# Kernel tuning notes

Measured on AMD Instinct MI355X. Metric: run time of the kernel, lower is better.

## Reference

```python
import jax, jax.numpy as jnp
import numpy as np

B, N_EX, N_KC, D_E, D_C, D_H = 32, 1024, 128, 64, 64, 64


def setup_inputs() -> dict:
    key = jax.random.key(0)
    ks = jax.random.split(key, 20)
    return {
        "h": jax.random.normal(ks[0], (B, N_KC, D_H), jnp.float32),
        "ex": jax.random.uniform(ks[1], (B, N_EX), jnp.float32),
        "su": jax.random.uniform(ks[2], (B,), jnp.float32),
        "ex_graph": jax.random.uniform(ks[3], (N_EX, N_KC), jnp.float32),
        "kc_gamma": jax.random.normal(ks[4], (N_KC, N_KC), jnp.float32),
        "W_ex": jax.random.normal(ks[5], (D_E, 2 * N_EX), jnp.float32) * 0.02,
        "W_kc": jax.random.normal(ks[6], (D_C, N_KC), jnp.float32) * 0.05,
        "tgru_wih": jax.random.normal(ks[7], (3 * D_H, D_E), jnp.float32) * 0.05,
        "tgru_whh": jax.random.normal(ks[8], (3 * D_H, D_H), jnp.float32) * 0.05,
        "tgru_bih": jax.random.normal(ks[9], (3 * D_H,), jnp.float32) * 0.05,
        "tgru_bhh": jax.random.normal(ks[10], (3 * D_H,), jnp.float32) * 0.05,
        "fpart_w": jax.random.normal(ks[11], (D_H, D_C + D_H), jnp.float32) * 0.05,
        "fpart_b": jax.random.normal(ks[12], (D_H,), jnp.float32) * 0.05,
        "ulin_w": jax.random.normal(ks[13], (D_H, D_H), jnp.float32) * 0.05,
        "ulin_b": jax.random.normal(ks[14], (D_H,), jnp.float32) * 0.05,
        "ugru_wih": jax.random.normal(ks[15], (3 * D_H, D_H), jnp.float32) * 0.05,
        "ugru_whh": jax.random.normal(ks[16], (3 * D_H, D_H), jnp.float32) * 0.05,
        "ugru_bih": jax.random.normal(ks[17], (3 * D_H,), jnp.float32) * 0.05,
        "ugru_bhh": jax.random.normal(ks[18], (3 * D_H,), jnp.float32) * 0.05,
    }


def _gru_cell(x, h, wih, whh, bih, bhh):
    # torch.nn.GRUCell: gates in order r, z, n
    gi = x @ wih.T + bih
    gh = h @ whh.T + bhh
    ir, iz, inn = jnp.split(gi, 3, axis=-1)
    hr, hz, hn = jnp.split(gh, 3, axis=-1)
    r = jax.nn.sigmoid(ir + hr)
    z = jax.nn.sigmoid(iz + hz)
    n = jnp.tanh(inn + r * hn)
    return (1.0 - z) * n + z * h


def reference(h, ex, su, ex_graph, kc_gamma, W_ex, W_kc,
              tgru_wih, tgru_whh, tgru_bih, tgru_bhh,
              fpart_w, fpart_b, ulin_w, ulin_b,
              ugru_wih, ugru_whh, ugru_bih, ugru_bhh):
    bsz, n_kc, d_h = h.shape
    kc_graph = jax.nn.sigmoid(kc_gamma)  # (n_kc, n_kc)

    # exercise embedding from [ex*su, ex*(1-su)]
    x_id = jnp.concatenate([ex * su[:, None], ex * (1.0 - su)[:, None]], axis=-1)  # (B, 2*n_ex)
    x = x_id @ W_ex.T  # (B, d_e)

    kci = ex @ ex_graph  # (B, n_kc)
    kci_flat = kci.reshape(bsz * n_kc, 1)

    # temporal GRU update, gated by kci
    x_rep = jnp.broadcast_to(x[:, None, :], (bsz, n_kc, x.shape[-1])).reshape(bsz * n_kc, -1)
    h_flat = h.reshape(bsz * n_kc, d_h)
    th = _gru_cell(x_rep, h_flat, tgru_wih, tgru_whh, tgru_bih, tgru_bhh)
    new_h = (1.0 - kci_flat) * h_flat + kci_flat * th  # (B*n_kc, d_h)

    delta_h = (new_h - h_flat).reshape(bsz, n_kc, d_h)

    # kc_embeddings(eye(n_kc)) == W_kc.T : (n_kc, d_c)
    e = W_kc.T
    # fpart(concat([delta_h_i, e_j])) split into the two weight blocks
    W_dh = fpart_w[:, :d_h]   # acts on delta_h
    W_e = fpart_w[:, d_h:]    # acts on e
    dpart = delta_h @ W_dh.T                      # (B, n_kc_i, d_h)
    epart = e @ W_e.T + fpart_b                   # (n_kc_j, d_h)
    pre = dpart[:, :, None, :] + epart[None, None, :, :]  # (B, i, j, d_h)
    partij = jax.nn.relu(pre)
    partij = partij * kc_graph[None, :, :, None] * kci[:, :, None, None]
    partj = jnp.sum(partij, axis=1)               # (B, n_kc_j, d_h)

    outj = jax.nn.relu(partj @ ulin_w.T + ulin_b).reshape(bsz * n_kc, d_h)
    kcj = (kci @ kc_graph).reshape(bsz * n_kc, 1)

    uh = _gru_cell(outj, new_h, ugru_wih, ugru_whh, ugru_bih, ugru_bhh)
    h_out = (1.0 - kcj) * new_h + kcj * uh
    return h_out.reshape(bsz, n_kc, d_h)
```

## Files before the change

### kernel.cpp

```cpp
#include <hip/hip_runtime.h>
#include <math.h>

#define NB  32
#define NKC 128
#define DH  64
#define NEX 1024
#define G3  192

#define XOFF    0
#define KCIOFF  2048
#define DPOFF   6144
#define FLAGOFF 268288
#define FLAGBYTE (FLAGOFF * 4)

#define S_WHH   0
#define S_WIH   6912
#define S_HT    13824
#define S_DLT   14848
#define S_XS    15872
#define S_KRED  15936
#define S_GIS   16448
#define S_BHH3  16640
#define S_KCIL  16832
#define S_DPT   0
#define S_FWB   8448
#define S_WKT   12800
#define S_PJS   13888
#define S_OUTJ  14912
#define S_EPS   15936
#define S_NEWH  17024
#define S_KCIF  18048
#define S_KCJ   18176
#define S_BIH   18192
#define S_BHH   18384
#define SM_SIZE 18576

__device__ __forceinline__ float sigf(float x) { return 1.0f / (1.0f + expf(-x)); }
__device__ __forceinline__ float dot4(float4 a, float4 b) {
    return fmaf(a.x, b.x, fmaf(a.y, b.y, fmaf(a.z, b.z, a.w * b.w)));
}

__global__ __launch_bounds__(512) void kF(
    const float* __restrict__ h, const float* __restrict__ ex,
    const float* __restrict__ su, const float* __restrict__ ex_graph,
    const float* __restrict__ kc_gamma,
    const float* __restrict__ W_ex, const float* __restrict__ W_kc,
    const float* __restrict__ tgru_wih, const float* __restrict__ tgru_whh,
    const float* __restrict__ tgru_bih, const float* __restrict__ tgru_bhh,
    const float* __restrict__ fpart_w, const float* __restrict__ fpart_b,
    const float* __restrict__ ulin_w, const float* __restrict__ ulin_b,
    const float* __restrict__ ugru_wih, const float* __restrict__ ugru_whh,
    const float* __restrict__ ugru_bih, const float* __restrict__ ugru_bhh,
    float* __restrict__ ws, float* __restrict__ out)
{
    int t = threadIdx.x, wave = t >> 6, lane = t & 63;
    int b  = blockIdx.x >> 3;
    int ck = blockIdx.x & 7;
    int i0 = ck * 16;

    __shared__ __align__(16) float sm[SM_SIZE];
    int* fx = (int*)(ws + FLAGOFF);
    int* fd = fx + 32;

    {
        float sub = su[b];
        const float* exb = ex + (size_t)b * NEX;
        float er[16];
        #pragma unroll
        for (int i = 0; i < 16; ++i) er[i] = exb[lane + i * 64];
        int d = ck * 8 + wave;
        const float* wr = W_ex + (size_t)d * (2 * NEX);
        float a1 = 0.f, a2 = 0.f;
        #pragma unroll
        for (int i = 0; i < 16; ++i) {
            int k = lane + i * 64;
            a1 = fmaf(er[i], wr[k], a1);
            a2 = fmaf(er[i], wr[NEX + k], a2);
        }
        float v = sub * a1 + (1.0f - sub) * a2;
        #pragma unroll
        for (int off = 32; off; off >>= 1) v += __shfl_down(v, off, 64);
        if (lane == 0) ws[XOFF + b * DH + d] = v;
    }
    __syncthreads();
    if (t == 0)
        __hip_atomic_fetch_add(fx + b, 1, __ATOMIC_RELEASE, __HIP_MEMORY_SCOPE_AGENT);

    {
        int i = t & 15, ks = t >> 4, kb = ks * 32;
        const float* exb = ex + (size_t)b * NEX;
        const float* eg = ex_graph + i0 + i;
        float a = 0.f;
        #pragma unroll 4
        for (int k = 0; k < 32; ++k)
            a = fmaf(exb[kb + k], eg[(size_t)(kb + k) * NKC], a);
        sm[S_KRED + t] = a;
    }
    {
        const float* hb = h + (size_t)(b * NKC + i0) * DH;
        for (int idx = t; idx < 16 * DH; idx += 512) sm[S_HT + idx] = hb[idx];
    }
    if (t < G3) sm[S_BHH3 + t] = tgru_bhh[t];
    __syncthreads();
    if (t < 16) {
        float s = 0.f;
        #pragma unroll
        for (int r = 0; r < 32; ++r) s += sm[S_KRED + r * 16 + t];
        sm[S_KCIL + t] = s;
        ws[KCIOFF + b * NKC + i0 + t] = s;
    }
    if (t == 0) {
        while (__hip_atomic_load(fx + b, __ATOMIC_ACQUIRE, __HIP_MEMORY_SCOPE_AGENT) < 8)
            __builtin_amdgcn_s_sleep(1);
    }
    __syncthreads();
    if (t < DH) sm[S_XS + t] = ws[XOFF + b * DH + t];

    float giA = (t < G3) ? tgru_bih[t] : 0.f;
    float ar[2], az[2], an[2];
    #pragma unroll
    for (int m = 0; m < 2; ++m) {
        ar[m] = sm[S_BHH3 + lane];
        az[m] = sm[S_BHH3 + 64 + lane];
        an[m] = sm[S_BHH3 + 128 + lane];
    }
    for (int ch = 0; ch < 2; ++ch) {
        __syncthreads();
        for (int idx = t; idx < G3 * 8; idx += 512) {
            int row = idx >> 3, q = idx & 7;
            *(float4*)&sm[S_WHH + row * 36 + 4 * q] =
                *(const float4*)&tgru_whh[row * DH + ch * 32 + 4 * q];
            *(float4*)&sm[S_WIH + row * 36 + 4 * q] =
                *(const float4*)&tgru_wih[row * DH + ch * 32 + 4 * q];
        }
        __syncthreads();
        if (t < G3) {
            #pragma unroll
            for (int q = 0; q < 8; ++q) {
                float4 wv = *(float4*)&sm[S_WIH + t * 36 + 4 * q];
                float4 xv = *(float4*)&sm[S_XS + ch * 32 + 4 * q];
                giA += dot4(wv, xv);
            }
        }
        #pragma unroll
        for (int q = 0; q < 8; ++q) {
            float4 wr = *(float4*)&sm[S_WHH + lane * 36 + 4 * q];
            float4 wz = *(float4*)&sm[S_WHH + (64 + lane) * 36 + 4 * q];
            float4 wn = *(float4*)&sm[S_WHH + (128 + lane) * 36 + 4 * q];
            int kb2 = ch * 32 + 4 * q;
            #pragma unroll
            for (int m = 0; m < 2; ++m) {
                float4 hk = *(float4*)&sm[S_HT + (wave * 2 + m) * DH + kb2];
                ar[m] += dot4(wr, hk);
                az[m] += dot4(wz, hk);
                an[m] += dot4(wn, hk);
            }
        }
    }
    if (t < G3) sm[S_GIS + t] = giA;
    __syncthreads();
    #pragma unroll
    for (int m = 0; m < 2; ++m) {
        int il = wave * 2 + m;
        float hval = sm[S_HT + il * DH + lane];
        float r = sigf(sm[S_GIS + lane] + ar[m]);
        float z = sigf(sm[S_GIS + 64 + lane] + az[m]);
        float n = tanhf(sm[S_GIS + 128 + lane] + r * an[m]);
        float th = (1.0f - z) * n + z * hval;
        float kv = sm[S_KCIL + il];
        float nh = (1.0f - kv) * hval + kv * th;
        sm[S_NEWH + il * DH + lane] = nh;
        sm[S_DLT + il * DH + lane] = kv * (th - hval);
    }
    __syncthreads();
    for (int idx = t; idx < 64 * 16; idx += 512) {
        int d = idx >> 4, q = idx & 15;
        *(float4*)&sm[S_WHH + d * 68 + 4 * q] = *(const float4*)&fpart_w[d * 128 + 4 * q];
    }
    __syncthreads();
    float acc[2] = {0.f, 0.f};
    #pragma unroll
    for (int q = 0; q < 16; ++q) {
        float4 w = *(float4*)&sm[S_WHH + lane * 68 + 4 * q];
        #pragma unroll
        for (int m = 0; m < 2; ++m) {
            float4 dv = *(float4*)&sm[S_DLT + (wave * 2 + m) * DH + 4 * q];
            acc[m] += dot4(w, dv);
        }
    }
    __syncthreads();
    #pragma unroll
    for (int m = 0; m < 2; ++m) sm[S_WIH + lane * 17 + wave * 2 + m] = acc[m];
    __syncthreads();
    for (int idx = t; idx < 1024; idx += 512) {
        int d = idx >> 4, il = idx & 15;
        ws[DPOFF + (size_t)b * 8192 + d * NKC + i0 + il] = sm[S_WIH + d * 17 + il];
    }
    __syncthreads();
    if (t == 0)
        __hip_atomic_fetch_add(fd + b, 1, __ATOMIC_RELEASE, __HIP_MEMORY_SCOPE_AGENT);

    for (int idx = t; idx < 64 * 16; idx += 512) {
        int d = idx >> 4, q = idx & 15;
        *(float4*)&sm[S_FWB + d * 68 + 4 * q] =
            *(const float4*)&fpart_w[d * 128 + 64 + 4 * q];
    }
    for (int idx = t; idx < 1024; idx += 512) {
        int cc = idx >> 4, jl = idx & 15;
        sm[S_WKT + jl * 68 + cc] = W_kc[(size_t)cc * NKC + i0 + jl];
    }
    if (t < G3) { sm[S_BIH + t] = ugru_bih[t]; sm[S_BHH + t] = ugru_bhh[t]; }
    if (t == 0) {
        while (__hip_atomic_load(fd + b, __ATOMIC_ACQUIRE, __HIP_MEMORY_SCOPE_AGENT) < 8)
            __builtin_amdgcn_s_sleep(1);
    }
    __syncthreads();
    {
        const float* dp = ws + DPOFF + (size_t)b * 8192;
        #pragma unroll
        for (int r = 0; r < 4; ++r) {
            int idx4 = t + r * 512;
            int d = idx4 >> 5, qi = idx4 & 31;
            *(float4*)&sm[S_DPT + d * 132 + 4 * qi] = *(const float4*)&dp[d * NKC + 4 * qi];
        }
    }
    if (t < NKC) sm[S_KCIF + t] = ws[KCIOFF + b * NKC + t];
    __syncthreads();
    #pragma unroll
    for (int r = 0; r < 2; ++r) {
        int idx = t + r * 512;
        int jl = idx >> 6, d = idx & 63;
        float a = fpart_b[d];
        #pragma unroll
        for (int q = 0; q < 16; ++q) {
            float4 fv = *(float4*)&sm[S_FWB + d * 68 + 4 * q];
            float4 wv = *(float4*)&sm[S_WKT + jl * 68 + 4 * q];
            a += dot4(fv, wv);
        }
        sm[S_EPS + jl * DH + d] = a;
    }
    __syncthreads();
    for (int idx = t; idx < 2048; idx += 512) {
        int i = idx >> 4, jl = idx & 15;
        sm[S_FWB + jl * 132 + i] = sm[S_KCIF + i] * sigf(kc_gamma[i * NKC + i0 + jl]);
    }
    __syncthreads();
    if (t < 16) {
        float s = 0.f;
        #pragma unroll
        for (int qi = 0; qi < 32; ++qi) {
            float4 v = *(float4*)&sm[S_FWB + t * 132 + 4 * qi];
            s += v.x + v.y + v.z + v.w;
        }
        sm[S_KCJ + t] = s;
    }
    float ep[2], pa[2];
    #pragma unroll
    for (int m = 0; m < 2; ++m) {
        ep[m] = sm[S_EPS + (wave * 2 + m) * DH + lane];
        pa[m] = 0.f;
    }
    for (int qi = 0; qi < 32; ++qi) {
        float4 dv = *(float4*)&sm[S_DPT + lane * 132 + 4 * qi];
        #pragma unroll
        for (int m = 0; m < 2; ++m) {
            float4 wv = *(float4*)&sm[S_FWB + (wave * 2 + m) * 132 + 4 * qi];
            pa[m] = fmaf(fmaxf(dv.x + ep[m], 0.f), wv.x, pa[m]);
            pa[m] = fmaf(fmaxf(dv.y + ep[m], 0.f), wv.y, pa[m]);
            pa[m] = fmaf(fmaxf(dv.z + ep[m], 0.f), wv.z, pa[m]);
            pa[m] = fmaf(fmaxf(dv.w + ep[m], 0.f), wv.w, pa[m]);
        }
    }
    #pragma unroll
    for (int m = 0; m < 2; ++m) sm[S_PJS + (wave * 2 + m) * DH + lane] = pa[m];
    __syncthreads();
    for (int idx = t; idx < 64 * 16; idx += 512) {
        int d = idx >> 4, q = idx & 15;
        *(float4*)&sm[d * 68 + 4 * q] = *(const float4*)&ulin_w[d * DH + 4 * q];
    }
    float ulb = ulin_b[lane];
    __syncthreads();
    float oa[2] = {ulb, ulb};
    #pragma unroll
    for (int q = 0; q < 16; ++q) {
        float4 uv = *(float4*)&sm[lane * 68 + 4 * q];
        #pragma unroll
        for (int m = 0; m < 2; ++m) {
            float4 pv = *(float4*)&sm[S_PJS + (wave * 2 + m) * DH + 4 * q];
            oa[m] += dot4(uv, pv);
        }
    }
    #pragma unroll
    for (int m = 0; m < 2; ++m)
        sm[S_OUTJ + (wave * 2 + m) * DH + lane] = fmaxf(oa[m], 0.f);
    float gir[2], giz[2], gin[2], ghr[2], ghz[2], ghn[2];
    #pragma unroll
    for (int m = 0; m < 2; ++m)
        gir[m] = giz[m] = gin[m] = ghr[m] = ghz[m] = ghn[m] = 0.f;
    for (int ch = 0; ch < 2; ++ch) {
        __syncthreads();
        for (int idx = t; idx < G3 * 8; idx += 512) {
            int row = idx >> 3, q = idx & 7;
            *(float4*)&sm[row * 36 + 4 * q] =
                *(const float4*)&ugru_wih[row * DH + ch * 32 + 4 * q];
            *(float4*)&sm[6912 + row * 36 + 4 * q] =
                *(const float4*)&ugru_whh[row * DH + ch * 32 + 4 * q];
        }
        __syncthreads();
        #pragma unroll
        for (int q = 0; q < 8; ++q) {
            float4 wir = *(float4*)&sm[lane * 36 + 4 * q];
            float4 wiz = *(float4*)&sm[(64 + lane) * 36 + 4 * q];
            float4 win = *(float4*)&sm[(128 + lane) * 36 + 4 * q];
            float4 wwr = *(float4*)&sm[6912 + lane * 36 + 4 * q];
            float4 wwz = *(float4*)&sm[6912 + (64 + lane) * 36 + 4 * q];
            float4 wwn = *(float4*)&sm[6912 + (128 + lane) * 36 + 4 * q];
            int kb2 = ch * 32 + 4 * q;
            #pragma unroll
            for (int m = 0; m < 2; ++m) {
                int jl = wave * 2 + m;
                float4 ov = *(float4*)&sm[S_OUTJ + jl * DH + kb2];
                float4 nv = *(float4*)&sm[S_NEWH + jl * DH + kb2];
                gir[m] += dot4(wir, ov);
                giz[m] += dot4(wiz, ov);
                gin[m] += dot4(win, ov);
                ghr[m] += dot4(wwr, nv);
                ghz[m] += dot4(wwz, nv);
                ghn[m] += dot4(wwn, nv);
            }
        }
    }
    #pragma unroll
    for (int m = 0; m < 2; ++m) {
        int jl = wave * 2 + m;
        float r = sigf(gir[m] + sm[S_BIH + lane] + ghr[m] + sm[S_BHH + lane]);
        float z = sigf(giz[m] + sm[S_BIH + 64 + lane] + ghz[m] + sm[S_BHH + 64 + lane]);
        float n = tanhf(gin[m] + sm[S_BIH + 128 + lane] +
                        r * (ghn[m] + sm[S_BHH + 128 + lane]));
        float nh = sm[S_NEWH + jl * DH + lane];
        float uh = (1.0f - z) * n + z * nh;
        float kj = sm[S_KCJ + jl];
        out[(size_t)(b * NKC + i0 + jl) * DH + lane] = (1.0f - kj) * nh + kj * uh;
    }
}

extern "C" void kernel_launch(void* const* d_in, const int* in_sizes, int n_in,
                              void* d_out, int out_size, void* d_ws, size_t ws_size,
                              hipStream_t stream) {
    const float* h        = (const float*)d_in[0];
    const float* ex       = (const float*)d_in[1];
    const float* su       = (const float*)d_in[2];
    const float* ex_graph = (const float*)d_in[3];
    const float* kc_gamma = (const float*)d_in[4];
    const float* W_ex     = (const float*)d_in[5];
    const float* W_kc     = (const float*)d_in[6];
    const float* tgru_wih = (const float*)d_in[7];
    const float* tgru_whh = (const float*)d_in[8];
    const float* tgru_bih = (const float*)d_in[9];
    const float* tgru_bhh = (const float*)d_in[10];
    const float* fpart_w  = (const float*)d_in[11];
    const float* fpart_b  = (const float*)d_in[12];
    const float* ulin_w   = (const float*)d_in[13];
    const float* ulin_b   = (const float*)d_in[14];
    const float* ugru_wih = (const float*)d_in[15];
    const float* ugru_whh = (const float*)d_in[16];
    const float* ugru_bih = (const float*)d_in[17];
    const float* ugru_bhh = (const float*)d_in[18];
    float* ws  = (float*)d_ws;
    float* out = (float*)d_out;

    hipMemsetAsync((char*)d_ws + FLAGBYTE, 0, 64 * sizeof(int), stream);
    hipLaunchKernelGGL(kF, dim3(256), dim3(512), 0, stream,
                       h, ex, su, ex_graph, kc_gamma, W_ex, W_kc,
                       tgru_wih, tgru_whh, tgru_bih, tgru_bhh,
                       fpart_w, fpart_b, ulin_w, ulin_b,
                       ugru_wih, ugru_whh, ugru_bih, ugru_bhh,
                       ws, out);
}
```

Measured before the change: 134.6 us.

## Split each batch into 16 blocks of 8 KCs, doubling grid size

The fused kernel now launches 512 blocks, each owning 8 knowledge components instead of 16, so every wave handles a single row rather than two. The change is meant to spread work across more of the MI355X's compute units and shorten each block's serial per-row work. It also moves kc_gamma, fpart_b and ulin_b loads ahead of the spin-wait, reworks the kci reduction into two stages, and compacts the shared-memory layout. In exchange, every block reloads all GRU and fpart weights, which doubles that global traffic. The per-batch spin barriers also now wait on 16 blocks, which requires all of them to be co-resident.

```diff
diff --git a/kernel.cpp b/kernel.cpp
--- a/kernel.cpp
+++ b/kernel.cpp
@@ -6,6 +6,8 @@
 #define DH  64
 #define NEX 1024
 #define G3  192
+#define CHK 8
+#define NCK 16
 
 #define XOFF    0
 #define KCIOFF  2048
@@ -14,33 +16,39 @@
 #define FLAGBYTE (FLAGOFF * 4)
 
 #define S_WHH   0
-#define S_WIH   6912
-#define S_HT    13824
-#define S_DLT   14848
-#define S_XS    15872
-#define S_KRED  15936
-#define S_GIS   16448
-#define S_BHH3  16640
-#define S_KCIL  16832
 #define S_DPT   0
+#define S_UL    0
+#define S_WIH36 0
+#define S_WHH36 6912
+#define S_WIH   8448
+#define S_DPTT  8448
 #define S_FWB   8448
+#define S_WJT   8448
 #define S_WKT   12800
-#define S_PJS   13888
-#define S_OUTJ  14912
-#define S_EPS   15936
-#define S_NEWH  17024
-#define S_KCIF  18048
-#define S_KCJ   18176
-#define S_BIH   18192
-#define S_BHH   18384
-#define SM_SIZE 18576
+#define S_HT    15360
+#define S_PJS   15360
+#define S_DLT   15872
+#define S_OUTJ  15872
+#define S_XS    16384
+#define S_KRED  16448
+#define S_EPS   16448
+#define S_KR2   16960
+#define S_GIS   17024
+#define S_BHH3  17216
+#define S_KCIL  17408
+#define S_NEWH  17424
+#define S_KCIF  17936
+#define S_KCJ   18064
+#define S_BIH   18080
+#define S_BHH   18272
+#define SM_SIZE 18464
 
 __device__ __forceinline__ float sigf(float x) { return 1.0f / (1.0f + expf(-x)); }
 __device__ __forceinline__ float dot4(float4 a, float4 b) {
     return fmaf(a.x, b.x, fmaf(a.y, b.y, fmaf(a.z, b.z, a.w * b.w)));
 }
 
-__global__ __launch_bounds__(512) void kF(
+__global__ __launch_bounds__(512, 4) void kF(
     const float* __restrict__ h, const float* __restrict__ ex,
     const float* __restrict__ su, const float* __restrict__ ex_graph,
     const float* __restrict__ kc_gamma,
@@ -54,21 +62,21 @@
     float* __restrict__ ws, float* __restrict__ out)
 {
     int t = threadIdx.x, wave = t >> 6, lane = t & 63;
-    int b  = blockIdx.x >> 3;
-    int ck = blockIdx.x & 7;
-    int i0 = ck * 16;
+    int b  = blockIdx.x >> 4;
+    int ck = blockIdx.x & 15;
+    int i0 = ck * CHK;
 
     __shared__ __align__(16) float sm[SM_SIZE];
     int* fx = (int*)(ws + FLAGOFF);
     int* fd = fx + 32;
 
-    {
+    if (wave < 4) {
         float sub = su[b];
         const float* exb = ex + (size_t)b * NEX;
         float er[16];
         #pragma unroll
         for (int i = 0; i < 16; ++i) er[i] = exb[lane + i * 64];
-        int d = ck * 8 + wave;
+        int d = ck * 4 + wave;
         const float* wr = W_ex + (size_t)d * (2 * NEX);
         float a1 = 0.f, a2 = 0.f;
         #pragma unroll
@@ -82,48 +90,51 @@
         for (int off = 32; off; off >>= 1) v += __shfl_down(v, off, 64);
         if (lane == 0) ws[XOFF + b * DH + d] = v;
     }
+    {
+        int i = t & 7, ks = t >> 3, kb = ks * 16;
+        const float* exb = ex + (size_t)b * NEX;
+        const float* eg = ex_graph + i0 + i;
+        float a0 = 0.f, a1 = 0.f;
+        #pragma unroll
+        for (int k = 0; k < 16; k += 2) {
+            a0 = fmaf(exb[kb + k],     eg[(size_t)(kb + k) * NKC], a0);
+            a1 = fmaf(exb[kb + k + 1], eg[(size_t)(kb + k + 1) * NKC], a1);
+        }
+        sm[S_KRED + t] = a0 + a1;
+    }
+    if (t < 128) {
+        const float* hb = h + (size_t)(b * NKC + i0) * DH;
+        *(float4*)&sm[S_HT + t * 4] = *(const float4*)&hb[t * 4];
+    }
+    if (t < G3) sm[S_BHH3 + t] = tgru_bhh[t];
     __syncthreads();
     if (t == 0)
         __hip_atomic_fetch_add(fx + b, 1, __ATOMIC_RELEASE, __HIP_MEMORY_SCOPE_AGENT);
-
-    {
-        int i = t & 15, ks = t >> 4, kb = ks * 32;
-        const float* exb = ex + (size_t)b * NEX;
-        const float* eg = ex_graph + i0 + i;
-        float a = 0.f;
-        #pragma unroll 4
-        for (int k = 0; k < 32; ++k)
-            a = fmaf(exb[kb + k], eg[(size_t)(kb + k) * NKC], a);
-        sm[S_KRED + t] = a;
-    }
-    {
-        const float* hb = h + (size_t)(b * NKC + i0) * DH;
-        for (int idx = t; idx < 16 * DH; idx += 512) sm[S_HT + idx] = hb[idx];
-    }
-    if (t < G3) sm[S_BHH3 + t] = tgru_bhh[t];
-    __syncthreads();
-    if (t < 16) {
+    if (t < 64) {
+        int i = t & 7, r = t >> 3;
         float s = 0.f;
         #pragma unroll
-        for (int r = 0; r < 32; ++r) s += sm[S_KRED + r * 16 + t];
+        for (int q = 0; q < 8; ++q) s += sm[S_KRED + (r * 8 + q) * 8 + i];
+        sm[S_KR2 + t] = s;
+    }
+    if (t < 8) {
+        float s = 0.f;
+        #pragma unroll
+        for (int q = 0; q < 8; ++q) s += sm[S_KR2 + q * 8 + t];
         sm[S_KCIL + t] = s;
         ws[KCIOFF + b * NKC + i0 + t] = s;
     }
     if (t == 0) {
-        while (__hip_atomic_load(fx + b, __ATOMIC_ACQUIRE, __HIP_MEMORY_SCOPE_AGENT) < 8)
+        while (__hip_atomic_load(fx + b, __ATOMIC_ACQUIRE, __HIP_MEMORY_SCOPE_AGENT) < NCK)
             __builtin_amdgcn_s_sleep(1);
     }
     __syncthreads();
     if (t < DH) sm[S_XS + t] = ws[XOFF + b * DH + t];
 
     float giA = (t < G3) ? tgru_bih[t] : 0.f;
-    float ar[2], az[2], an[2];
-    #pragma unroll
-    for (int m = 0; m < 2; ++m) {
-        ar[m] = sm[S_BHH3 + lane];
-        az[m] = sm[S_BHH3 + 64 + lane];
-        an[m] = sm[S_BHH3 + 128 + lane];
-    }
+    float ar = sm[S_BHH3 + lane];
+    float az = sm[S_BHH3 + 64 + lane];
+    float an = sm[S_BHH3 + 128 + lane];
     for (int ch = 0; ch < 2; ++ch) {
         __syncthreads();
         for (int idx = t; idx < G3 * 8; idx += 512) {
@@ -136,41 +147,31 @@
         __syncthreads();
         if (t < G3) {
             #pragma unroll
-            for (int q = 0; q < 8; ++q) {
-                float4 wv = *(float4*)&sm[S_WIH + t * 36 + 4 * q];
-                float4 xv = *(float4*)&sm[S_XS + ch * 32 + 4 * q];
-                giA += dot4(wv, xv);
-            }
+            for (int q = 0; q < 8; ++q)
+                giA += dot4(*(float4*)&sm[S_WIH + t * 36 + 4 * q],
+                            *(float4*)&sm[S_XS + ch * 32 + 4 * q]);
         }
         #pragma unroll
         for (int q = 0; q < 8; ++q) {
-            float4 wr = *(float4*)&sm[S_WHH + lane * 36 + 4 * q];
-            float4 wz = *(float4*)&sm[S_WHH + (64 + lane) * 36 + 4 * q];
-            float4 wn = *(float4*)&sm[S_WHH + (128 + lane) * 36 + 4 * q];
             int kb2 = ch * 32 + 4 * q;
-            #pragma unroll
-            for (int m = 0; m < 2; ++m) {
-                float4 hk = *(float4*)&sm[S_HT + (wave * 2 + m) * DH + kb2];
-                ar[m] += dot4(wr, hk);
-                az[m] += dot4(wz, hk);
-                an[m] += dot4(wn, hk);
-            }
+            float4 hk = *(float4*)&sm[S_HT + wave * DH + kb2];
+            ar += dot4(*(float4*)&sm[S_WHH + lane * 36 + 4 * q], hk);
+            az += dot4(*(float4*)&sm[S_WHH + (64 + lane) * 36 + 4 * q], hk);
+            an += dot4(*(float4*)&sm[S_WHH + (128 + lane) * 36 + 4 * q], hk);
         }
     }
     if (t < G3) sm[S_GIS + t] = giA;
     __syncthreads();
-    #pragma unroll
-    for (int m = 0; m < 2; ++m) {
-        int il = wave * 2 + m;
-        float hval = sm[S_HT + il * DH + lane];
-        float r = sigf(sm[S_GIS + lane] + ar[m]);
-        float z = sigf(sm[S_GIS + 64 + lane] + az[m]);
-        float n = tanhf(sm[S_GIS + 128 + lane] + r * an[m]);
+    {
+        float hval = sm[S_HT + wave * DH + lane];
+        float r = sigf(sm[S_GIS + lane] + ar);
+        float z = sigf(sm[S_GIS + 64 + lane] + az);
+        float n = tanhf(sm[S_GIS + 128 + lane] + r * an);
         float th = (1.0f - z) * n + z * hval;
-        float kv = sm[S_KCIL + il];
+        float kv = sm[S_KCIL + wave];
         float nh = (1.0f - kv) * hval + kv * th;
-        sm[S_NEWH + il * DH + lane] = nh;
-        sm[S_DLT + il * DH + lane] = kv * (th - hval);
+        sm[S_NEWH + wave * DH + lane] = nh;
+        sm[S_DLT + wave * DH + lane] = kv * (th - hval);
     }
     __syncthreads();
     for (int idx = t; idx < 64 * 16; idx += 512) {
@@ -178,40 +179,38 @@
         *(float4*)&sm[S_WHH + d * 68 + 4 * q] = *(const float4*)&fpart_w[d * 128 + 4 * q];
     }
     __syncthreads();
-    float acc[2] = {0.f, 0.f};
+    float acc = 0.f;
     #pragma unroll
-    for (int q = 0; q < 16; ++q) {
-        float4 w = *(float4*)&sm[S_WHH + lane * 68 + 4 * q];
-        #pragma unroll
-        for (int m = 0; m < 2; ++m) {
-            float4 dv = *(float4*)&sm[S_DLT + (wave * 2 + m) * DH + 4 * q];
-            acc[m] += dot4(w, dv);
-        }
-    }
-    __syncthreads();
-    #pragma unroll
-    for (int m = 0; m < 2; ++m) sm[S_WIH + lane * 17 + wave * 2 + m] = acc[m];
-    __syncthreads();
-    for (int idx = t; idx < 1024; idx += 512) {
-        int d = idx >> 4, il = idx & 15;
-        ws[DPOFF + (size_t)b * 8192 + d * NKC + i0 + il] = sm[S_WIH + d * 17 + il];
+    for (int q = 0; q < 16; ++q)
+        acc += dot4(*(float4*)&sm[S_WHH + lane * 68 + 4 * q],
+                    *(float4*)&sm[S_DLT + wave * DH + 4 * q]);
+    sm[S_DPTT + lane * 9 + wave] = acc;
+    __syncthreads();
+    {
+        int d = t >> 3, il = t & 7;
+        ws[DPOFF + (size_t)b * 8192 + d * NKC + i0 + il] = sm[S_DPTT + d * 9 + il];
     }
     __syncthreads();
     if (t == 0)
         __hip_atomic_fetch_add(fd + b, 1, __ATOMIC_RELEASE, __HIP_MEMORY_SCOPE_AGENT);
 
+    int ic = t >> 3, jc = t & 7;
+    float g0  = kc_gamma[(size_t)ic * NKC + i0 + jc];
+    float g1  = kc_gamma[(size_t)(ic + 64) * NKC + i0 + jc];
+    float fpb = fpart_b[t & 63];
+    float ulb = ulin_b[lane];
     for (int idx = t; idx < 64 * 16; idx += 512) {
         int d = idx >> 4, q = idx & 15;
         *(float4*)&sm[S_FWB + d * 68 + 4 * q] =
             *(const float4*)&fpart_w[d * 128 + 64 + 4 * q];
     }
-    for (int idx = t; idx < 1024; idx += 512) {
-        int cc = idx >> 4, jl = idx & 15;
-        sm[S_WKT + jl * 68 + cc] = W_kc[(size_t)cc * NKC + i0 + jl];
+    {
+        int c = t >> 3, jl = t & 7;
+        sm[S_WKT + jl * 68 + c] = W_kc[(size_t)c * NKC + i0 + jl];
     }
     if (t < G3) { sm[S_BIH + t] = ugru_bih[t]; sm[S_BHH + t] = ugru_bhh[t]; }
     if (t == 0) {
-        while (__hip_atomic_load(fd + b, __ATOMIC_ACQUIRE, __HIP_MEMORY_SCOPE_AGENT) < 8)
+        while (__hip_atomic_load(fd + b, __ATOMIC_ACQUIRE, __HIP_MEMORY_SCOPE_AGENT) < NCK)
             __builtin_amdgcn_s_sleep(1);
     }
     __syncthreads();
@@ -226,121 +225,83 @@
     }
     if (t < NKC) sm[S_KCIF + t] = ws[KCIOFF + b * NKC + t];
     __syncthreads();
-    #pragma unroll
-    for (int r = 0; r < 2; ++r) {
-        int idx = t + r * 512;
-        int jl = idx >> 6, d = idx & 63;
-        float a = fpart_b[d];
-        #pragma unroll
-        for (int q = 0; q < 16; ++q) {
-            float4 fv = *(float4*)&sm[S_FWB + d * 68 + 4 * q];
-            float4 wv = *(float4*)&sm[S_WKT + jl * 68 + 4 * q];
-            a += dot4(fv, wv);
-        }
+    {
+        int jl = t >> 6, d = t & 63;
+        float a = fpb;
+        #pragma unroll
+        for (int q = 0; q < 16; ++q)
+            a += dot4(*(float4*)&sm[S_FWB + d * 68 + 4 * q],
+                      *(float4*)&sm[S_WKT + jl * 68 + 4 * q]);
         sm[S_EPS + jl * DH + d] = a;
     }
     __syncthreads();
-    for (int idx = t; idx < 2048; idx += 512) {
-        int i = idx >> 4, jl = idx & 15;
-        sm[S_FWB + jl * 132 + i] = sm[S_KCIF + i] * sigf(kc_gamma[i * NKC + i0 + jl]);
-    }
-    __syncthreads();
-    if (t < 16) {
+    sm[S_WJT + jc * 132 + ic]      = sm[S_KCIF + ic]      * sigf(g0);
+    sm[S_WJT + jc * 132 + ic + 64] = sm[S_KCIF + ic + 64] * sigf(g1);
+    __syncthreads();
+    if (t < 8) {
         float s = 0.f;
         #pragma unroll
         for (int qi = 0; qi < 32; ++qi) {
-            float4 v = *(float4*)&sm[S_FWB + t * 132 + 4 * qi];
+            float4 v = *(float4*)&sm[S_WJT + t * 132 + 4 * qi];
             s += v.x + v.y + v.z + v.w;
         }
         sm[S_KCJ + t] = s;
     }
-    float ep[2], pa[2];
-    #pragma unroll
-    for (int m = 0; m < 2; ++m) {
-        ep[m] = sm[S_EPS + (wave * 2 + m) * DH + lane];
-        pa[m] = 0.f;
-    }
+    float ep = sm[S_EPS + wave * DH + lane], pa = 0.f;
     for (int qi = 0; qi < 32; ++qi) {
         float4 dv = *(float4*)&sm[S_DPT + lane * 132 + 4 * qi];
-        #pragma unroll
-        for (int m = 0; m < 2; ++m) {
-            float4 wv = *(float4*)&sm[S_FWB + (wave * 2 + m) * 132 + 4 * qi];
-            pa[m] = fmaf(fmaxf(dv.x + ep[m], 0.f), wv.x, pa[m]);
-            pa[m] = fmaf(fmaxf(dv.y + ep[m], 0.f), wv.y, pa[m]);
-            pa[m] = fmaf(fmaxf(dv.z + ep[m], 0.f), wv.z, pa[m]);
-            pa[m] = fmaf(fmaxf(dv.w + ep[m], 0.f), wv.w, pa[m]);
-        }
-    }
-    #pragma unroll
-    for (int m = 0; m < 2; ++m) sm[S_PJS + (wave * 2 + m) * DH + lane] = pa[m];
+        float4 wv = *(float4*)&sm[S_WJT + wave * 132 + 4 * qi];
+        pa = fmaf(fmaxf(dv.x + ep, 0.f), wv.x, pa);
+        pa = fmaf(fmaxf(dv.y + ep, 0.f), wv.y, pa);
+        pa = fmaf(fmaxf(dv.z + ep, 0.f), wv.z, pa);
+        pa = fmaf(fmaxf(dv.w + ep, 0.f), wv.w, pa);
+    }
+    sm[S_PJS + wave * DH + lane] = pa;
     __syncthreads();
     for (int idx = t; idx < 64 * 16; idx += 512) {
         int d = idx >> 4, q = idx & 15;
-        *(float4*)&sm[d * 68 + 4 * q] = *(const float4*)&ulin_w[d * DH + 4 * q];
-    }
-    float ulb = ulin_b[lane];
-    __syncthreads();
-    float oa[2] = {ulb, ulb};
+        *(float4*)&sm[S_UL + d * 68 + 4 * q] = *(const float4*)&ulin_w[d * DH + 4 * q];
+    }
+    __syncthreads();
+    float oa = ulb;
     #pragma unroll
-    for (int q = 0; q < 16; ++q) {
-        float4 uv = *(float4*)&sm[lane * 68 + 4 * q];
-        #pragma unroll
-        for (int m = 0; m < 2; ++m) {
-            float4 pv = *(float4*)&sm[S_PJS + (wave * 2 + m) * DH + 4 * q];
-            oa[m] += dot4(uv, pv);
-        }
-    }
-    #pragma unroll
-    for (int m = 0; m < 2; ++m)
-        sm[S_OUTJ + (wave * 2 + m) * DH + lane] = fmaxf(oa[m], 0.f);
-    float gir[2], giz[2], gin[2], ghr[2], ghz[2], ghn[2];
-    #pragma unroll
-    for (int m = 0; m < 2; ++m)
-        gir[m] = giz[m] = gin[m] = ghr[m] = ghz[m] = ghn[m] = 0.f;
+    for (int q = 0; q < 16; ++q)
+        oa += dot4(*(float4*)&sm[S_UL + lane * 68 + 4 * q],
+                   *(float4*)&sm[S_PJS + wave * DH + 4 * q]);
+    sm[S_OUTJ + wave * DH + lane] = fmaxf(oa, 0.f);
+    float gir = 0.f, giz = 0.f, gin = 0.f, ghr = 0.f, ghz = 0.f, ghn = 0.f;
     for (int ch = 0; ch < 2; ++ch) {
         __syncthreads();
         for (int idx = t; idx < G3 * 8; idx += 512) {
             int row = idx >> 3, q = idx & 7;
-            *(float4*)&sm[row * 36 + 4 * q] =
+            *(float4*)&sm[S_WIH36 + row * 36 + 4 * q] =
                 *(const float4*)&ugru_wih[row * DH + ch * 32 + 4 * q];
-            *(float4*)&sm[6912 + row * 36 + 4 * q] =
+            *(float4*)&sm[S_WHH36 + row * 36 + 4 * q] =
                 *(const float4*)&ugru_whh[row * DH + ch * 32 + 4 * q];
         }
         __syncthreads();
         #pragma unroll
         for (int q = 0; q < 8; ++q) {
-            float4 wir = *(float4*)&sm[lane * 36 + 4 * q];
-            float4 wiz = *(float4*)&sm[(64 + lane) * 36 + 4 * q];
-            float4 win = *(float4*)&sm[(128 + lane) * 36 + 4 * q];
-            float4 wwr = *(float4*)&sm[6912 + lane * 36 + 4 * q];
-            float4 wwz = *(float4*)&sm[6912 + (64 + lane) * 36 + 4 * q];
-            float4 wwn = *(float4*)&sm[6912 + (128 + lane) * 36 + 4 * q];
             int kb2 = ch * 32 + 4 * q;
-            #pragma unroll
-            for (int m = 0; m < 2; ++m) {
-                int jl = wave * 2 + m;
-                float4 ov = *(float4*)&sm[S_OUTJ + jl * DH + kb2];
-                float4 nv = *(float4*)&sm[S_NEWH + jl * DH + kb2];
-                gir[m] += dot4(wir, ov);
-                giz[m] += dot4(wiz, ov);
-                gin[m] += dot4(win, ov);
-                ghr[m] += dot4(wwr, nv);
-                ghz[m] += dot4(wwz, nv);
-                ghn[m] += dot4(wwn, nv);
-            }
-        }
-    }
-    #pragma unroll
-    for (int m = 0; m < 2; ++m) {
-        int jl = wave * 2 + m;
-        float r = sigf(gir[m] + sm[S_BIH + lane] + ghr[m] + sm[S_BHH + lane]);
-        float z = sigf(giz[m] + sm[S_BIH + 64 + lane] + ghz[m] + sm[S_BHH + 64 + lane]);
-        float n = tanhf(gin[m] + sm[S_BIH + 128 + lane] +
-                        r * (ghn[m] + sm[S_BHH + 128 + lane]));
-        float nh = sm[S_NEWH + jl * DH + lane];
+            float4 ov = *(float4*)&sm[S_OUTJ + wave * DH + kb2];
+            float4 nv = *(float4*)&sm[S_NEWH + wave * DH + kb2];
+            gir += dot4(*(float4*)&sm[S_WIH36 + lane * 36 + 4 * q], ov);
+            giz += dot4(*(float4*)&sm[S_WIH36 + (64 + lane) * 36 + 4 * q], ov);
+            gin += dot4(*(float4*)&sm[S_WIH36 + (128 + lane) * 36 + 4 * q], ov);
+            ghr += dot4(*(float4*)&sm[S_WHH36 + lane * 36 + 4 * q], nv);
+            ghz += dot4(*(float4*)&sm[S_WHH36 + (64 + lane) * 36 + 4 * q], nv);
+            ghn += dot4(*(float4*)&sm[S_WHH36 + (128 + lane) * 36 + 4 * q], nv);
+        }
+    }
+    {
+        float r = sigf(gir + sm[S_BIH + lane] + ghr + sm[S_BHH + lane]);
+        float z = sigf(giz + sm[S_BIH + 64 + lane] + ghz + sm[S_BHH + 64 + lane]);
+        float n = tanhf(gin + sm[S_BIH + 128 + lane] +
+                        r * (ghn + sm[S_BHH + 128 + lane]));
+        float nh = sm[S_NEWH + wave * DH + lane];
         float uh = (1.0f - z) * n + z * nh;
-        float kj = sm[S_KCJ + jl];
-        out[(size_t)(b * NKC + i0 + jl) * DH + lane] = (1.0f - kj) * nh + kj * uh;
+        float kj = sm[S_KCJ + wave];
+        out[(size_t)(b * NKC + i0 + wave) * DH + lane] = (1.0f - kj) * nh + kj * uh;
     }
 }
 
@@ -370,7 +331,7 @@
     float* out = (float*)d_out;
 
     hipMemsetAsync((char*)d_ws + FLAGBYTE, 0, 64 * sizeof(int), stream);
-    hipLaunchKernelGGL(kF, dim3(256), dim3(512), 0, stream,
+    hipLaunchKernelGGL(kF, dim3(512), dim3(512), 0, stream,
                        h, ex, su, ex_graph, kc_gamma, W_ex, W_kc,
                        tgru_wih, tgru_whh, tgru_bih, tgru_bhh,
                        fpart_w, fpart_b, ulin_w, ulin_b,
```

New measurement: 257.9 us. 91.5% more time.
